# Optimization experiments

Hardware: AMD Instinct MI355X
Metric: run time of the kernel (lower is better)

The kernel has to match this reference:

```python
import jax, jax.numpy as jnp
import numpy as np
from jax import lax

EPS = 1e-5
DIM = 96      # channels = dim
KS = 96       # kernel_size == H == W
GROUPS = 8
BATCH = 4
FFN_F = 2.66

# relative index table: emb[c, i, j] = rel[c, i - j + KS - 1]
_REL_IDX = (np.arange(KS)[:, None] - np.arange(KS)[None, :] + KS - 1).reshape(-1)


def _bn(x, g, b, ax):
    """BatchNorm (training-mode batch statistics) over all axes except `ax`."""
    axes = tuple(i for i in range(x.ndim) if i != ax)
    m = x.mean(axes, keepdims=True)
    v = x.var(axes, keepdims=True)
    sh = [1] * x.ndim
    sh[ax] = -1
    return (x - m) / jnp.sqrt(v + EPS) * g.reshape(sh) + b.reshape(sh)


def _ln(x, w, b):
    """WithBias LayerNorm over channel dim of NCHW (per-pixel over C)."""
    m = x.mean(1, keepdims=True)
    v = x.var(1, keepdims=True)
    return (x - m) / jnp.sqrt(v + EPS) * w[None, :, None, None] + b[None, :, None, None]


def _axial(x, wqkv, gq, bq, rel, gs, bs, go, bo, width):
    # x: (N, C, H, W)
    xp = x.transpose(0, 2, 1, 3) if width else x.transpose(0, 3, 1, 2)
    N, Wd, C, L = xp.shape
    gp = C // GROUPS  # group_planes
    xb = xp.reshape(N * Wd, C, L)
    qkv = _bn(jnp.einsum('oc,bcl->bol', wqkv, xb), gq, bq, 1)
    qkv = qkv.reshape(N * Wd, GROUPS, 2 * gp, L)
    q, k, v = qkv[:, :, :gp // 2], qkv[:, :, gp // 2:gp], qkv[:, :, gp:]
    emb = rel[:, _REL_IDX].reshape(2 * gp, L, L)
    qe, ke, ve = emb[:gp // 2], emb[gp // 2:gp], emb[gp:]
    qk = jnp.einsum('bgci,bgcj->bgij', q, k)
    qr = jnp.einsum('bgci,cij->bgij', q, qe)
    kr = jnp.einsum('bgci,cij->bgij', k, ke).transpose(0, 1, 3, 2)
    sim = _bn(jnp.concatenate([qk, qr, kr], 1), gs, bs, 1)
    sim = sim.reshape(N * Wd, 3, GROUPS, L, L).sum(1)
    sim = jax.nn.softmax(sim, axis=3)
    sv = jnp.einsum('bgij,bgcj->bgci', sim, v)
    sve = jnp.einsum('bgij,cij->bgci', sim, ve)
    out = _bn(jnp.concatenate([sv, sve], -1).reshape(N * Wd, 2 * C, L), go, bo, 1)
    out = out.reshape(N, Wd, C, 2, L).sum(3)
    return out.transpose(0, 2, 1, 3) if width else out.transpose(0, 2, 3, 1)


def _ffn(x, win, wdw, wout):
    h = jnp.einsum('oc,bchw->bohw', win, x)
    h = lax.conv_general_dilated(h, wdw, (1, 1), 'SAME',
                                 dimension_numbers=('NCHW', 'OIHW', 'NCHW'),
                                 feature_group_count=h.shape[1])
    x1, x2 = jnp.split(h, 2, axis=1)
    return jnp.einsum('oc,bchw->bohw', wout, jax.nn.gelu(x1, approximate=False) * x2)


def setup_inputs() -> dict:
    key = jax.random.key(0)
    ks = jax.random.split(key, 8)
    dim, gp = DIM, DIM // GROUPS
    hid = int(dim * FFN_F)
    f = jax.random.normal
    d = {'x': f(ks[0], (BATCH, dim, KS, KS), jnp.float32)}
    d['ln1_w'] = jnp.ones(dim); d['ln1_b'] = jnp.zeros(dim)
    for p, i in (('h_', 1), ('w_', 2)):
        k1, k2 = jax.random.split(ks[i])
        d[p + 'wqkv'] = f(k1, (2 * dim, dim), jnp.float32) * float(np.sqrt(1.0 / dim))
        d[p + 'gqkv'] = jnp.ones(2 * dim); d[p + 'bqkv'] = jnp.zeros(2 * dim)
        d[p + 'rel'] = f(k2, (2 * gp, 2 * KS - 1), jnp.float32) * float(np.sqrt(1.0 / gp))
        d[p + 'gsim'] = jnp.ones(3 * GROUPS); d[p + 'bsim'] = jnp.zeros(3 * GROUPS)
        d[p + 'gout'] = jnp.ones(2 * dim); d[p + 'bout'] = jnp.zeros(2 * dim)
    d['ln2_w'] = jnp.ones(dim); d['ln2_b'] = jnp.zeros(dim)
    d['ffn_win'] = f(ks[3], (2 * hid, dim), jnp.float32) * float(np.sqrt(1.0 / dim))
    d['ffn_wdw'] = f(ks[4], (2 * hid, 1, 3, 3), jnp.float32) * 0.1
    d['ffn_wout'] = f(ks[5], (dim, hid), jnp.float32) * float(np.sqrt(1.0 / hid))
    return d


def reference(x, ln1_w, ln1_b,
              h_wqkv, h_gqkv, h_bqkv, h_rel, h_gsim, h_bsim, h_gout, h_bout,
              w_wqkv, w_gqkv, w_bqkv, w_rel, w_gsim, w_bsim, w_gout, w_bout,
              ln2_w, ln2_b, ffn_win, ffn_wdw, ffn_wout):
    y = _ln(x, ln1_w, ln1_b)
    y = _axial(y, h_wqkv, h_gqkv, h_bqkv, h_rel, h_gsim, h_bsim, h_gout, h_bout, False)
    y = _axial(y, w_wqkv, w_gqkv, w_bqkv, w_rel, w_gsim, w_bsim, w_gout, w_bout, True)
    x = x + y
    x = x + _ffn(_ln(x, ln2_w, ln2_b), ffn_win, ffn_wdw, ffn_wout)
    return x
```

## Files before the change

### kernel.cpp

```cpp
#include <hip/hip_runtime.h>
#include <hip/hip_bf16.h>
#include <math.h>

using bf16 = __hip_bfloat16;

#define NB 4
#define C_ 96
#define NPIX 36864
#define IMG 9216
#define CH_ST 9216
#define N_ST 884736
#define HID 255
#define EPSF 1e-5f
#define TOT 3538944

__global__ __launch_bounds__(256) void ln_kernel(const float* __restrict__ X,
                                                 float* __restrict__ Y,
                                                 const float* __restrict__ w,
                                                 const float* __restrict__ b) {
  __shared__ float red[2][4][64];
  __shared__ float wb[192];
  int tid = threadIdx.x;
  if (tid < 192) wb[tid] = (tid < 96) ? w[tid] : b[tid - 96];
  int cq = tid >> 6, px = tid & 63;
  int pix = blockIdx.x * 64 + px;
  int n = pix / IMG, p = pix % IMG;
  const float* xp = X + (long)n * N_ST + (long)(cq * 24) * CH_ST + p;
  float xr[24];
  float s = 0.f, sq = 0.f;
  #pragma unroll
  for (int k = 0; k < 24; k++) {
    float v = xp[(long)k * CH_ST];
    xr[k] = v; s += v; sq += v * v;
  }
  red[0][cq][px] = s; red[1][cq][px] = sq;
  __syncthreads();
  float S  = red[0][0][px] + red[0][1][px] + red[0][2][px] + red[0][3][px];
  float SQ = red[1][0][px] + red[1][1][px] + red[1][2][px] + red[1][3][px];
  float m = S * (1.f / C_);
  float r = rsqrtf(fmaxf(SQ * (1.f / C_) - m * m, 0.f) + EPSF);
  float* yp = Y + (long)n * N_ST + (long)(cq * 24) * CH_ST + p;
  #pragma unroll
  for (int k = 0; k < 24; k++)
    yp[(long)k * CH_ST] = (xr[k] - m) * r * wb[cq * 24 + k] + wb[96 + cq * 24 + k];
}

__global__ void trans_kernel(const float* __restrict__ Y0, float* __restrict__ Y0C) {
  __shared__ float T[32][33];
  int nc = blockIdx.z; int n = nc / C_, c = nc % C_;
  int h0 = blockIdx.x * 32, w0 = blockIdx.y * 32;
  int tx = threadIdx.x, ty = threadIdx.y;
  const float* src = Y0 + (long)n * N_ST + (long)c * CH_ST;
  for (int r = 0; r < 4; r++)
    T[ty + 8 * r][tx] = src[(h0 + ty + 8 * r) * 96 + w0 + tx];
  __syncthreads();
  float* dst = Y0C + (long)c * NPIX + (long)n * IMG;
  for (int r = 0; r < 4; r++)
    dst[(w0 + ty + 8 * r) * 96 + h0 + tx] = T[tx][ty + 8 * r];
}

template<int TM, int TN, int EPI>
__global__ __launch_bounds__(256) void gemm_kernel(
    const float* __restrict__ A, const float* __restrict__ B,
    float* __restrict__ Cout, int M, int K, int NperZ,
    long bCstride, long bZstride, int batch,
    const float* __restrict__ X1, float* __restrict__ OutF) {
  constexpr int NT = TN / 16;
  constexpr int RT = TM / 16;
  __shared__ float As[32][TM];
  __shared__ float Bs[32][TN + 4];
  const int tx = threadIdx.x, ty = threadIdx.y;
  const int tid = ty * 16 + tx;
  const int m0 = blockIdx.y * TM;
  const int q0 = blockIdx.x * TN;
  const int z  = blockIdx.z;
  const float* Bz = B + (long)z * bZstride;
  float acc[RT][NT];
  #pragma unroll
  for (int a = 0; a < RT; a++)
    #pragma unroll
    for (int b = 0; b < NT; b++) acc[a][b] = 0.f;

  for (int kk = 0; kk < K; kk += 32) {
    #pragma unroll
    for (int it = 0; it < (32 * TM) / 256; it++) {
      int i = tid + it * 256;
      int c = i / TM, r = i % TM;
      int mm = m0 + r, kc = kk + c;
      As[c][r] = (mm < M && kc < K) ? A[(long)mm * K + kc] : 0.f;
    }
    #pragma unroll
    for (int it = 0; it < (32 * TN) / 256; it++) {
      int i = tid + it * 256;
      int c = i / TN, q = i % TN;
      int kc = kk + c;
      Bs[c][q] = (kc < K) ? Bz[(long)kc * bCstride + q0 + q] : 0.f;
    }
    __syncthreads();
    for (int kc = 0; kc < 32; kc++) {
      float av[RT];
      if constexpr (RT % 4 == 0) {
        #pragma unroll
        for (int u = 0; u < RT / 4; u++) {
          float4 a4 = *(const float4*)&As[kc][ty * RT + 4 * u];
          av[4 * u] = a4.x; av[4 * u + 1] = a4.y; av[4 * u + 2] = a4.z; av[4 * u + 3] = a4.w;
        }
      } else {
        #pragma unroll
        for (int u = 0; u < RT / 2; u++) {
          float2 a2 = *(const float2*)&As[kc][ty * RT + 2 * u];
          av[2 * u] = a2.x; av[2 * u + 1] = a2.y;
        }
      }
      float bv[NT];
      #pragma unroll
      for (int v4 = 0; v4 < NT / 4; v4++) {
        float4 b4 = *(const float4*)&Bs[kc][v4 * 64 + tx * 4];
        bv[v4 * 4] = b4.x; bv[v4 * 4 + 1] = b4.y; bv[v4 * 4 + 2] = b4.z; bv[v4 * 4 + 3] = b4.w;
      }
      #pragma unroll
      for (int a = 0; a < RT; a++)
        #pragma unroll
        for (int b = 0; b < NT; b++)
          acc[a][b] = fmaf(av[a], bv[b], acc[a][b]);
    }
    __syncthreads();
  }
  const long oStride = (long)NperZ * gridDim.z;
  if (EPI == 0) {
    #pragma unroll
    for (int a = 0; a < RT; a++) {
      int mm = m0 + ty * RT + a;
      if (mm < M) {
        float* dst = Cout + (long)mm * oStride + (long)z * NperZ + q0;
        #pragma unroll
        for (int v4 = 0; v4 < NT / 4; v4++)
          *(float4*)(dst + v4 * 64 + tx * 4) =
              make_float4(acc[a][v4 * 4], acc[a][v4 * 4 + 1],
                          acc[a][v4 * 4 + 2], acc[a][v4 * 4 + 3]);
      }
    }
  } else {
    #pragma unroll
    for (int a = 0; a < RT; a++) {
      int mm = m0 + ty * RT + a;
      if (mm < M) {
        #pragma unroll
        for (int v4 = 0; v4 < NT / 4; v4++) {
          int Q = q0 + v4 * 64 + tx * 4;
          int n = batch + z + Q / IMG, p = Q % IMG;
          long base = (long)n * N_ST + (long)mm * CH_ST + p;
          #pragma unroll
          for (int b = 0; b < 4; b++)
            OutF[base + b] = acc[a][v4 * 4 + b] + X1[base + b];
        }
      }
    }
  }
}

__global__ __launch_bounds__(1024) void rowstat_kernel(const float* __restrict__ D,
                                                       const float* __restrict__ g,
                                                       const float* __restrict__ b,
                                                       float2* __restrict__ aff) {
  int o = blockIdx.x;
  const float4* p = (const float4*)(D + (long)o * NPIX);
  float s = 0.f, sq = 0.f;
  for (int i = threadIdx.x; i < NPIX / 4; i += 1024) {
    float4 v = p[i];
    s  += v.x + v.y + v.z + v.w;
    sq += v.x * v.x + v.y * v.y + v.z * v.z + v.w * v.w;
  }
  for (int off = 32; off; off >>= 1) { s += __shfl_down(s, off); sq += __shfl_down(sq, off); }
  __shared__ float ss[16], ssq[16];
  int wv = threadIdx.x >> 6, lane = threadIdx.x & 63;
  if (lane == 0) { ss[wv] = s; ssq[wv] = sq; }
  __syncthreads();
  if (threadIdx.x == 0) {
    float S = 0.f, SQ = 0.f;
    #pragma unroll
    for (int i = 0; i < 16; i++) { S += ss[i]; SQ += ssq[i]; }
    float m = S / (float)NPIX;
    float var = fmaxf(SQ / (float)NPIX - m * m, 0.f);
    float sc = g[o] * rsqrtf(var + EPSF);
    aff[o] = make_float2(sc, b[o] - m * sc);
  }
}

__global__ void relstat_kernel(const float* __restrict__ relp, float* __restrict__ tbl) {
  int i = threadIdx.x;
  if (i >= 96) return;
  int side = blockIdx.x / 27, row = blockIdx.x % 27;
  const float* base = relp + side * 6 * 191;
  float* T = tbl + side * 27 * 96;
  if (row < 6) {
    float s = 0.f;
    for (int d = 0; d < 96; d++) s += base[row * 191 + i + d];
    T[row * 96 + i] = s;
  } else {
    int p = row - 6, c = 0;
    while (p >= 6 - c) { p -= 6 - c; c++; }
    int c2 = c + p;
    float s = 0.f;
    for (int d = 0; d < 96; d++) s += base[c * 191 + i + d] * base[c2 * 191 + i + d];
    T[576 + (row - 6) * 96 + i] = s;
  }
}

__global__ __launch_bounds__(256) void simstat2_kernel(const float* __restrict__ QKV,
                                                       const float2* __restrict__ aff,
                                                       const float* __restrict__ tbl,
                                                       float* __restrict__ stats) {
  int g = blockIdx.x & 7, chunk = blockIdx.x >> 3;
  int bbg = threadIdx.x >> 5, lane = threadIdx.x & 31;
  int bb = chunk * 8 + bbg;
  const float* Aq = tbl;
  const float* Wq = tbl + 6 * 96;
  const float* Ak = tbl + 27 * 96;
  const float* Wk = tbl + 27 * 96 + 6 * 96;
  float Sq[6] = {}, Sk[6] = {}, Gq[21] = {}, Gk[21] = {};
  float lq = 0.f, lsq = 0.f, lk = 0.f, lsk = 0.f;
  #pragma unroll
  for (int ii = 0; ii < 3; ii++) {
    int i = lane + 32 * ii;
    float qv[6], kv[6];
    #pragma unroll
    for (int c = 0; c < 6; c++) {
      int oq = g * 24 + c, ok = g * 24 + 6 + c;
      float2 a = aff[oq], b2 = aff[ok];
      qv[c] = QKV[(long)oq * NPIX + bb * 96 + i] * a.x + a.y;
      kv[c] = QKV[(long)ok * NPIX + bb * 96 + i] * b2.x + b2.y;
      Sq[c] += qv[c]; Sk[c] += kv[c];
      lq = fmaf(qv[c], Aq[c * 96 + i], lq);
      lk = fmaf(kv[c], Ak[c * 96 + i], lk);
    }
    int p = 0;
    #pragma unroll
    for (int c = 0; c < 6; c++)
      #pragma unroll
      for (int c2 = c; c2 < 6; c2++, p++) {
        float f = (c == c2) ? 1.f : 2.f;
        float pq = qv[c] * qv[c2], pk = kv[c] * kv[c2];
        Gq[p] += pq; Gk[p] += pk;
        lsq = fmaf(pq * f, Wq[p * 96 + i], lsq);
        lsk = fmaf(pk * f, Wk[p * 96 + i], lsk);
      }
  }
  #pragma unroll
  for (int off = 16; off; off >>= 1) {
    #pragma unroll
    for (int c = 0; c < 6; c++) { Sq[c] += __shfl_down(Sq[c], off, 32); Sk[c] += __shfl_down(Sk[c], off, 32); }
    #pragma unroll
    for (int p = 0; p < 21; p++) { Gq[p] += __shfl_down(Gq[p], off, 32); Gk[p] += __shfl_down(Gk[p], off, 32); }
    lq += __shfl_down(lq, off, 32);  lsq += __shfl_down(lsq, off, 32);
    lk += __shfl_down(lk, off, 32);  lsk += __shfl_down(lsk, off, 32);
  }
  __shared__ float red[6];
  if (threadIdx.x < 6) red[threadIdx.x] = 0.f;
  __syncthreads();
  if (lane == 0) {
    float sqk = 0.f, sqk2 = 0.f;
    #pragma unroll
    for (int c = 0; c < 6; c++) sqk += Sq[c] * Sk[c];
    int p = 0;
    #pragma unroll
    for (int c = 0; c < 6; c++)
      #pragma unroll
      for (int c2 = c; c2 < 6; c2++, p++)
        sqk2 += ((c == c2) ? 1.f : 2.f) * Gq[p] * Gk[p];
    atomicAdd(&red[0], sqk); atomicAdd(&red[3], sqk2);
    atomicAdd(&red[1], lq);  atomicAdd(&red[4], lsq);
    atomicAdd(&red[2], lk);  atomicAdd(&red[5], lsk);
  }
  __syncthreads();
  if (threadIdx.x < 3) {
    atomicAdd(&stats[(threadIdx.x * 8 + g) * 2 + 0], red[threadIdx.x]);
    atomicAdd(&stats[(threadIdx.x * 8 + g) * 2 + 1], red[threadIdx.x + 3]);
  }
}

__global__ void simfin_kernel(const float* __restrict__ stats,
                              const float* __restrict__ gsim,
                              float* __restrict__ scale) {
  int t = threadIdx.x;
  if (t < 24) {
    float cnt = 384.f * 9216.f;
    float m = stats[t * 2] / cnt;
    float var = fmaxf(stats[t * 2 + 1] / cnt - m * m, 0.f);
    scale[t] = gsim[t] * rsqrtf(var + EPSF);
  }
}

__global__ __launch_bounds__(256) void attn_kernel(const float* __restrict__ QKV,
                                                   const float2* __restrict__ aff,
                                                   const float* __restrict__ relp,
                                                   const float* __restrict__ sscale,
                                                   float* __restrict__ OutPre) {
  int blk = blockIdx.x;
  int bb = blk >> 3, g = blk & 7;
  __shared__ float qF[6][96];
  __shared__ float kF[6][96];
  __shared__ float vF[12][96];
  __shared__ float rl[24 * 191];
  __shared__ float P[32][100];
  int tid = threadIdx.x;
  float s0 = sscale[g], s1 = sscale[8 + g], s2 = sscale[16 + g];
  for (int i = tid; i < 288; i += 256) {
    int half = i / 144, r = i % 144;
    int c = r / 24, qd = r % 24;
    int o = g * 24 + half * 6 + c;
    float2 a = aff[o];
    float4 v = *(const float4*)(QKV + (long)o * NPIX + bb * 96 + qd * 4);
    float4 w = make_float4(v.x * a.x + a.y, v.y * a.x + a.y,
                           v.z * a.x + a.y, v.w * a.x + a.y);
    if (half == 0) *(float4*)&qF[c][qd * 4] = w;
    else           *(float4*)&kF[c][qd * 4] = w;
  }
  for (int i = tid; i < 288; i += 256) {
    int c = i / 24, qd = i % 24;
    int o = g * 24 + 12 + c;
    float2 a = aff[o];
    float4 v = *(const float4*)(QKV + (long)o * NPIX + bb * 96 + qd * 4);
    *(float4*)&vF[c][qd * 4] = make_float4(v.x * a.x + a.y, v.y * a.x + a.y,
                                           v.z * a.x + a.y, v.w * a.x + a.y);
  }
  for (int i = tid; i < 1146; i += 256) {
    int e = i * 4;
    float4 v = *(const float4*)(relp + e);
    float4 w;
    w.x = v.x * ((e + 0) < 1146 ? s1 : (e + 0) < 2292 ? s2 : 1.f);
    w.y = v.y * ((e + 1) < 1146 ? s1 : (e + 1) < 2292 ? s2 : 1.f);
    w.z = v.z * ((e + 2) < 1146 ? s1 : (e + 2) < 2292 ? s2 : 1.f);
    w.w = v.w * ((e + 3) < 1146 ? s1 : (e + 3) < 2292 ? s2 : 1.f);
    *(float4*)&rl[e] = w;
  }
  __syncthreads();
  int hw = tid >> 5, l32 = tid & 31;
  float kreg[6][3];
  #pragma unroll
  for (int c = 0; c < 6; c++)
    #pragma unroll
    for (int j = 0; j < 3; j++) kreg[c][j] = kF[c][l32 * 3 + j];
  for (int iq = 0; iq < 3; iq++) {
    int i0 = iq * 32;
    {
      int til = hw * 4;
      int ti = i0 + til;
      int tj = l32 * 3;
      int d0 = ti - tj + 93;
      int e0 = tj - ti + 92;
      float ap[4][3] = {};
      #pragma unroll
      for (int c = 0; c < 6; c++) {
        float4 q4 = *(const float4*)&qF[c][ti];
        float qv[4] = {q4.x, q4.y, q4.z, q4.w};
        float kv0[3], rq[6], rk[6];
        #pragma unroll
        for (int j = 0; j < 3; j++) kv0[j] = s0 * kreg[c][j];
        #pragma unroll
        for (int u = 0; u < 6; u++) { rq[u] = rl[c * 191 + d0 + u]; rk[u] = rl[(6 + c) * 191 + e0 + u]; }
        #pragma unroll
        for (int ii = 0; ii < 4; ii++)
          #pragma unroll
          for (int jj = 0; jj < 3; jj++) {
            ap[ii][jj] = fmaf(qv[ii], kv0[jj], ap[ii][jj]);
            ap[ii][jj] = fmaf(qv[ii], rq[ii - jj + 2], ap[ii][jj]);
            ap[ii][jj] = fmaf(kreg[c][jj], rk[jj - ii + 3], ap[ii][jj]);
          }
      }
      #pragma unroll
      for (int ii = 0; ii < 4; ii++)
        #pragma unroll
        for (int jj = 0; jj < 3; jj++)
          P[til + ii][l32 * 3 + jj] = ap[ii][jj];
    }
    __syncthreads();
    {
      int wv = tid >> 6, rloc = (tid >> 3) & 7, l8 = tid & 7;
      int r = wv * 8 + rloc;
      float* Pr = &P[r][l8 * 12];
      float4 v0 = *(const float4*)(Pr);
      float4 v1 = *(const float4*)(Pr + 4);
      float4 v2 = *(const float4*)(Pr + 8);
      float mx = fmaxf(fmaxf(fmaxf(v0.x, v0.y), fmaxf(v0.z, v0.w)),
                 fmaxf(fmaxf(fmaxf(v1.x, v1.y), fmaxf(v1.z, v1.w)),
                       fmaxf(fmaxf(v2.x, v2.y), fmaxf(v2.z, v2.w))));
      #pragma unroll
      for (int off = 4; off; off >>= 1) mx = fmaxf(mx, __shfl_xor(mx, off, 8));
      v0 = make_float4(__expf(v0.x - mx), __expf(v0.y - mx), __expf(v0.z - mx), __expf(v0.w - mx));
      v1 = make_float4(__expf(v1.x - mx), __expf(v1.y - mx), __expf(v1.z - mx), __expf(v1.w - mx));
      v2 = make_float4(__expf(v2.x - mx), __expf(v2.y - mx), __expf(v2.z - mx), __expf(v2.w - mx));
      float s = v0.x + v0.y + v0.z + v0.w + v1.x + v1.y + v1.z + v1.w
              + v2.x + v2.y + v2.z + v2.w;
      #pragma unroll
      for (int off = 4; off; off >>= 1) s += __shfl_xor(s, off, 8);
      *(float4*)(Pr)     = v0;
      *(float4*)(Pr + 4) = v1;
      *(float4*)(Pr + 8) = v2;
      if (l8 == 0) P[r][96] = 1.f / s;
    }
    __syncthreads();
    {
      int orr0 = hw * 3;
      float acc3[3] = {};
      for (int jq = 0; jq < 24; jq++) {
        int j0 = jq * 4;
        float4 pv = *(const float4*)&P[l32][j0];
        #pragma unroll
        for (int u = 0; u < 3; u++) {
          int orr = orr0 + u, cc = orr >> 1;
          if ((orr & 1) == 0) {
            float4 vv = *(const float4*)&vF[cc][j0];
            acc3[u] += pv.x * vv.x + pv.y * vv.y + pv.z * vv.z + pv.w * vv.w;
          } else {
            const float* rv = &rl[(12 + cc) * 191];
            int bse = (i0 + l32) - j0 + 92;
            float f0 = rv[bse], f1 = rv[bse + 1], f2 = rv[bse + 2], f3 = rv[bse + 3];
            acc3[u] += pv.w * f0 + pv.z * f1 + pv.y * f2 + pv.x * f3;
          }
        }
      }
      float ri = P[l32][96];
      #pragma unroll
      for (int u = 0; u < 3; u++)
        OutPre[(long)(g * 24 + orr0 + u) * NPIX + bb * 96 + i0 + l32] = acc3[u] * ri;
    }
    __syncthreads();
  }
}

__global__ void apply1_kernel(const float* __restrict__ OutPre,
                              const float2* __restrict__ aff,
                              float* __restrict__ Y1) {
  __shared__ float T[32][33];
  int z = blockIdx.z; int n = z / C_, cf = z % C_;
  int h0 = blockIdx.x * 32, w0 = blockIdx.y * 32;
  int tx = threadIdx.x, ty = threadIdx.y;
  float2 a0 = aff[2 * cf], a1 = aff[2 * cf + 1];
  const float* r0 = OutPre + (long)(2 * cf) * NPIX + (long)n * IMG;
  const float* r1 = OutPre + (long)(2 * cf + 1) * NPIX + (long)n * IMG;
  for (int r = 0; r < 4; r++) {
    int w = w0 + ty + 8 * r;
    int idx = w * 96 + h0 + tx;
    T[ty + 8 * r][tx] = (r0[idx] * a0.x + a0.y) + (r1[idx] * a1.x + a1.y);
  }
  __syncthreads();
  float* dst = Y1 + (long)n * N_ST + (long)cf * CH_ST;
  for (int r = 0; r < 4; r++)
    dst[(h0 + ty + 8 * r) * 96 + w0 + tx] = T[tx][ty + 8 * r];
}

__global__ __launch_bounds__(256) void apl2_kernel(const float* __restrict__ OutPre,
                                                   const float2* __restrict__ aff,
                                                   const float* __restrict__ X,
                                                   const float* __restrict__ w,
                                                   const float* __restrict__ b,
                                                   float* __restrict__ X1out,
                                                   float* __restrict__ Yln) {
  __shared__ float red[2][4][64];
  __shared__ float2 affs[192];
  __shared__ float wb[192];
  int tid = threadIdx.x;
  if (tid < 192) { affs[tid] = aff[tid]; wb[tid] = (tid < 96) ? w[tid] : b[tid - 96]; }
  __syncthreads();
  int cq = tid >> 6, px = tid & 63;
  int pix = blockIdx.x * 64 + px;
  int n = pix / IMG, p = pix % IMG;
  const float* o0p = OutPre + (long)n * IMG + p;
  const float* xp = X + (long)n * N_ST + (long)(cq * 24) * CH_ST + p;
  float vr[24];
  float s = 0.f, sq = 0.f;
  #pragma unroll
  for (int k = 0; k < 24; k++) {
    int c = cq * 24 + k;
    float2 a0 = affs[2 * c], a1 = affs[2 * c + 1];
    float o0 = o0p[(long)(2 * c) * NPIX];
    float o1 = o0p[(long)(2 * c + 1) * NPIX];
    float v = o0 * a0.x + a0.y + o1 * a1.x + a1.y + xp[(long)k * CH_ST];
    vr[k] = v; s += v; sq += v * v;
  }
  red[0][cq][px] = s; red[1][cq][px] = sq;
  __syncthreads();
  float S  = red[0][0][px] + red[0][1][px] + red[0][2][px] + red[0][3][px];
  float SQ = red[1][0][px] + red[1][1][px] + red[1][2][px] + red[1][3][px];
  float m = S * (1.f / C_);
  float r = rsqrtf(fmaxf(SQ * (1.f / C_) - m * m, 0.f) + EPSF);
  float* x1p = X1out + (long)n * N_ST + (long)(cq * 24) * CH_ST + p;
  float* yp  = Yln   + (long)n * N_ST + (long)(cq * 24) * CH_ST + p;
  #pragma unroll
  for (int k = 0; k < 24; k++) {
    x1p[(long)k * CH_ST] = vr[k];
    int c = cq * 24 + k;
    yp[(long)k * CH_ST] = (vr[k] - m) * r * wb[c] + wb[96 + c];
  }
}

__global__ __launch_bounds__(256) void dwglu_kernel(const float* __restrict__ H,
                                                    const float* __restrict__ Wdw,
                                                    float* __restrict__ Gout) {
  int idx = blockIdx.x * 256 + threadIdx.x;
  if (idx >= HID * IMG) return;
  int c = idx / IMG;
  int p = idx % IMG, y = p / 96, x = p % 96;
  const float* h1 = H + (long)c * IMG;
  const float* h2 = H + (long)(c + HID) * IMG;
  const float* w1 = Wdw + c * 9;
  const float* w2 = Wdw + (c + HID) * 9;
  float acc1 = 0.f, acc2 = 0.f;
  #pragma unroll
  for (int dy = -1; dy <= 1; dy++) {
    int yy = y + dy; if (yy < 0 || yy >= 96) continue;
    #pragma unroll
    for (int dx = -1; dx <= 1; dx++) {
      int xx = x + dx; if (xx < 0 || xx >= 96) continue;
      int wi = (dy + 1) * 3 + dx + 1;
      acc1 = fmaf(h1[yy * 96 + xx], w1[wi], acc1);
      acc2 = fmaf(h2[yy * 96 + xx], w2[wi], acc2);
    }
  }
  float ge = 0.5f * acc1 * (1.f + erff(acc1 * 0.70710678118654752f));
  Gout[idx] = ge * acc2;
}

__global__ __launch_bounds__(256) void dwglu4_kernel(const float* __restrict__ H,
                                                     const float* __restrict__ Wdw,
                                                     float* __restrict__ Gout) {
  int idx = blockIdx.x * 256 + threadIdx.x;
  if (idx >= HID * IMG * NB) return;
  int c = idx / (IMG * NB);
  int rem = idx % (IMG * NB);
  int nb = rem / IMG;
  int p = rem % IMG, y = p / 96, x = p % 96;
  const float* h1 = H + (long)c * (IMG * NB) + (long)nb * IMG;
  const float* h2 = H + (long)(c + HID) * (IMG * NB) + (long)nb * IMG;
  const float* w1 = Wdw + c * 9;
  const float* w2 = Wdw + (c + HID) * 9;
  float acc1 = 0.f, acc2 = 0.f;
  #pragma unroll
  for (int dy = -1; dy <= 1; dy++) {
    int yy = y + dy; if (yy < 0 || yy >= 96) continue;
    #pragma unroll
    for (int dx = -1; dx <= 1; dx++) {
      int xx = x + dx; if (xx < 0 || xx >= 96) continue;
      int wi = (dy + 1) * 3 + dx + 1;
      acc1 = fmaf(h1[yy * 96 + xx], w1[wi], acc1);
      acc2 = fmaf(h2[yy * 96 + xx], w2[wi], acc2);
    }
  }
  float ge = 0.5f * acc1 * (1.f + erff(acc1 * 0.70710678118654752f));
  Gout[(long)nb * 2350080 + (long)c * IMG + p] = ge * acc2;
}

extern "C" void kernel_launch(void* const* d_in, const int* in_sizes, int n_in,
                              void* d_out, int out_size, void* d_ws, size_t ws_size,
                              hipStream_t stream) {
  const float* x       = (const float*)d_in[0];
  const float* ln1w    = (const float*)d_in[1];
  const float* ln1b    = (const float*)d_in[2];
  const float* h_wqkv  = (const float*)d_in[3];
  const float* h_gqkv  = (const float*)d_in[4];
  const float* h_bqkv  = (const float*)d_in[5];
  const float* h_rel   = (const float*)d_in[6];
  const float* h_gsim  = (const float*)d_in[7];
  const float* h_gout  = (const float*)d_in[9];
  const float* h_bout  = (const float*)d_in[10];
  const float* w_wqkv  = (const float*)d_in[11];
  const float* w_gqkv  = (const float*)d_in[12];
  const float* w_bqkv  = (const float*)d_in[13];
  const float* w_rel   = (const float*)d_in[14];
  const float* w_gsim  = (const float*)d_in[15];
  const float* w_gout  = (const float*)d_in[17];
  const float* w_bout  = (const float*)d_in[18];
  const float* ln2w    = (const float*)d_in[19];
  const float* ln2b    = (const float*)d_in[20];
  const float* ffn_win = (const float*)d_in[21];
  const float* ffn_wdw = (const float*)d_in[22];
  const float* ffn_wout= (const float*)d_in[23];
  float* out = (float*)d_out;

  float* ws = (float*)d_ws;
  float* P = ws;
  float* Q = ws + 3538944;
  float* R = ws + 7077888;
  float* S = ws + 14155776;
  float* Gall = R;
  float* Hbuf = ws + 16478208;
  const size_t base_need = (21233664ull + 8192ull) * 4ull;
  const size_t big_need  = (35278848ull + 8192ull) * 4ull;
  if (ws_size < base_need) return;
  const bool batched = (ws_size >= big_need);
  float* stats = batched ? (ws + 35278848) : (ws + 21233664);

  float2* qkv_aff = (float2*)stats;
  float2* out_aff = (float2*)(stats + 384);
  float*  sim_st  = stats + 768;
  float*  sim_sc  = stats + 864;
  float*  tbl     = stats + 1024;

  hipMemsetAsync(sim_st, 0, 96 * sizeof(float), stream);

  dim3 b256(256), b1616(16, 16), b328(32, 8);

  ln_kernel<<<576, b256, 0, stream>>>(x, P, ln1w, ln1b);
  trans_kernel<<<dim3(3, 3, 384), b328, 0, stream>>>(P, Q);

  gemm_kernel<96, 128, 0><<<dim3(288, 2, 1), b1616, 0, stream>>>(h_wqkv, Q, R,
      192, 96, 36864, 36864L, 0L, 0, nullptr, nullptr);
  rowstat_kernel<<<192, 1024, 0, stream>>>(R, h_gqkv, h_bqkv, qkv_aff);
  relstat_kernel<<<54, 96, 0, stream>>>(h_rel, tbl);
  simstat2_kernel<<<384, b256, 0, stream>>>(R, qkv_aff, tbl, sim_st);
  simfin_kernel<<<1, 32, 0, stream>>>(sim_st, h_gsim, sim_sc);
  attn_kernel<<<3072, b256, 0, stream>>>(R, qkv_aff, h_rel, sim_sc, S);
  rowstat_kernel<<<192, 1024, 0, stream>>>(S, h_gout, h_bout, out_aff);
  apply1_kernel<<<dim3(3, 3, 384), b328, 0, stream>>>(S, out_aff, P);

  gemm_kernel<96, 128, 0><<<dim3(72, 2, 4), b1616, 0, stream>>>(w_wqkv, P, R,
      192, 96, 9216, 9216L, 884736L, 0, nullptr, nullptr);
  rowstat_kernel<<<192, 1024, 0, stream>>>(R, w_gqkv, w_bqkv, qkv_aff);
  relstat_kernel<<<54, 96, 0, stream>>>(w_rel, tbl);
  simstat2_kernel<<<384, b256, 0, stream>>>(R, qkv_aff, tbl, sim_st + 48);
  simfin_kernel<<<1, 32, 0, stream>>>(sim_st + 48, w_gsim, sim_sc + 24);
  attn_kernel<<<3072, b256, 0, stream>>>(R, qkv_aff, w_rel, sim_sc + 24, S);
  rowstat_kernel<<<192, 1024, 0, stream>>>(S, w_gout, w_bout, out_aff);
  apl2_kernel<<<576, b256, 0, stream>>>(S, out_aff, x, ln2w, ln2b, P, Q);

  if (batched) {
    gemm_kernel<128, 64, 0><<<dim3(144, 4, 4), b1616, 0, stream>>>(ffn_win, Q, Hbuf,
        510, 96, 9216, 9216L, 884736L, 0, nullptr, nullptr);
    dwglu4_kernel<<<36720, b256, 0, stream>>>(Hbuf, ffn_wdw, Gall);
  } else {
    for (int n = 0; n < NB; n++) {
      gemm_kernel<128, 64, 0><<<dim3(144, 4, 1), b1616, 0, stream>>>(ffn_win, Q + (long)n * N_ST, Hbuf,
          510, 96, 9216, 9216L, 0L, 0, nullptr, nullptr);
      dwglu_kernel<<<9180, b256, 0, stream>>>(Hbuf, ffn_wdw, Gall + (long)n * 2350080);
    }
  }
  gemm_kernel<96, 64, 1><<<dim3(144, 1, 4), b1616, 0, stream>>>(ffn_wout, Gall, nullptr,
      96, 255, 9216, 9216L, 2350080L, 0, P, out);
}
```

Measured before the change: 852.9 us.

## Fuse QKV batchnorm statistics into GEMM epilogue and drop finalize kernels

The QKV GEMM epilogue now reduces per-row sum and sum of squares across lanes and atomically accumulates them, which removes the two rowstat passes over the 192x36864 QKV buffer. The simstat and attention kernels compute the BN affine and similarity scales inline, so the simfin kernels are gone as well. apply1 zeroes the sum buffer between the two axial passes, and a single memset clears the stats area. The cost is extra shuffles and global atomics in the GEMM, plus a one-pass variance formula that is less numerically robust.

```diff
diff --git a/kernel.cpp b/kernel.cpp
--- a/kernel.cpp
+++ b/kernel.cpp
@@ -13,6 +13,7 @@
 #define HID 255
 #define EPSF 1e-5f
 #define TOT 3538944
+#define RNPIX (1.f / 36864.f)
 
 __global__ __launch_bounds__(256) void ln_kernel(const float* __restrict__ X,
                                                  float* __restrict__ Y,
@@ -59,12 +60,13 @@
     dst[(w0 + ty + 8 * r) * 96 + h0 + tx] = T[tx][ty + 8 * r];
 }
 
-template<int TM, int TN, int EPI>
+template<int TM, int TN, int EPI, int STATS>
 __global__ __launch_bounds__(256) void gemm_kernel(
     const float* __restrict__ A, const float* __restrict__ B,
     float* __restrict__ Cout, int M, int K, int NperZ,
     long bCstride, long bZstride, int batch,
-    const float* __restrict__ X1, float* __restrict__ OutF) {
+    const float* __restrict__ X1, float* __restrict__ OutF,
+    float* __restrict__ rsum) {
   constexpr int NT = TN / 16;
   constexpr int RT = TM / 16;
   __shared__ float As[32][TM];
@@ -154,6 +156,23 @@
           for (int b = 0; b < 4; b++)
             OutF[base + b] = acc[a][v4 * 4 + b] + X1[base + b];
         }
+      }
+    }
+  }
+  if (STATS) {
+    #pragma unroll
+    for (int a = 0; a < RT; a++) {
+      int mm = m0 + ty * RT + a;
+      float s = 0.f, sq = 0.f;
+      #pragma unroll
+      for (int b = 0; b < NT; b++) { float v = acc[a][b]; s += v; sq += v * v; }
+      #pragma unroll
+      for (int off = 8; off; off >>= 1) {
+        s += __shfl_down(s, off, 16); sq += __shfl_down(sq, off, 16);
+      }
+      if (tx == 0 && mm < M) {
+        atomicAdd(&rsum[mm], s);
+        atomicAdd(&rsum[192 + mm], sq);
       }
     }
   }
@@ -208,7 +227,9 @@
 }
 
 __global__ __launch_bounds__(256) void simstat2_kernel(const float* __restrict__ QKV,
-                                                       const float2* __restrict__ aff,
+                                                       const float* __restrict__ qsum,
+                                                       const float* __restrict__ gq,
+                                                       const float* __restrict__ bq,
                                                        const float* __restrict__ tbl,
                                                        float* __restrict__ stats) {
   int g = blockIdx.x & 7, chunk = blockIdx.x >> 3;
@@ -218,6 +239,17 @@
   const float* Wq = tbl + 6 * 96;
   const float* Ak = tbl + 27 * 96;
   const float* Wk = tbl + 27 * 96 + 6 * 96;
+  float qa[6], qb[6], ka[6], kb[6];
+  #pragma unroll
+  for (int c = 0; c < 6; c++) {
+    int oq = g * 24 + c, ok = g * 24 + 6 + c;
+    float m1 = qsum[oq] * RNPIX;
+    float v1 = fmaxf(qsum[192 + oq] * RNPIX - m1 * m1, 0.f);
+    qa[c] = gq[oq] * rsqrtf(v1 + EPSF); qb[c] = bq[oq] - m1 * qa[c];
+    float m2 = qsum[ok] * RNPIX;
+    float v2 = fmaxf(qsum[192 + ok] * RNPIX - m2 * m2, 0.f);
+    ka[c] = gq[ok] * rsqrtf(v2 + EPSF); kb[c] = bq[ok] - m2 * ka[c];
+  }
   float Sq[6] = {}, Sk[6] = {}, Gq[21] = {}, Gk[21] = {};
   float lq = 0.f, lsq = 0.f, lk = 0.f, lsk = 0.f;
   #pragma unroll
@@ -227,9 +259,8 @@
     #pragma unroll
     for (int c = 0; c < 6; c++) {
       int oq = g * 24 + c, ok = g * 24 + 6 + c;
-      float2 a = aff[oq], b2 = aff[ok];
-      qv[c] = QKV[(long)oq * NPIX + bb * 96 + i] * a.x + a.y;
-      kv[c] = QKV[(long)ok * NPIX + bb * 96 + i] * b2.x + b2.y;
+      qv[c] = QKV[(long)oq * NPIX + bb * 96 + i] * qa[c] + qb[c];
+      kv[c] = QKV[(long)ok * NPIX + bb * 96 + i] * ka[c] + kb[c];
       Sq[c] += qv[c]; Sk[c] += kv[c];
       lq = fmaf(qv[c], Aq[c * 96 + i], lq);
       lk = fmaf(kv[c], Ak[c * 96 + i], lk);
@@ -279,22 +310,13 @@
   }
 }
 
-__global__ void simfin_kernel(const float* __restrict__ stats,
-                              const float* __restrict__ gsim,
-                              float* __restrict__ scale) {
-  int t = threadIdx.x;
-  if (t < 24) {
-    float cnt = 384.f * 9216.f;
-    float m = stats[t * 2] / cnt;
-    float var = fmaxf(stats[t * 2 + 1] / cnt - m * m, 0.f);
-    scale[t] = gsim[t] * rsqrtf(var + EPSF);
-  }
-}
-
 __global__ __launch_bounds__(256) void attn_kernel(const float* __restrict__ QKV,
-                                                   const float2* __restrict__ aff,
+                                                   const float* __restrict__ qsum,
+                                                   const float* __restrict__ gq,
+                                                   const float* __restrict__ bq,
                                                    const float* __restrict__ relp,
-                                                   const float* __restrict__ sscale,
+                                                   const float* __restrict__ simst,
+                                                   const float* __restrict__ gsim,
                                                    float* __restrict__ OutPre) {
   int blk = blockIdx.x;
   int bb = blk >> 3, g = blk & 7;
@@ -303,13 +325,28 @@
   __shared__ float vF[12][96];
   __shared__ float rl[24 * 191];
   __shared__ float P[32][100];
+  __shared__ float2 aff_s[24];
   int tid = threadIdx.x;
-  float s0 = sscale[g], s1 = sscale[8 + g], s2 = sscale[16 + g];
+  const float rc = 1.f / 3538944.f;
+  float m0s = simst[2 * g] * rc;
+  float s0 = gsim[g] * rsqrtf(fmaxf(simst[2 * g + 1] * rc - m0s * m0s, 0.f) + EPSF);
+  float m1s = simst[2 * (8 + g)] * rc;
+  float s1 = gsim[8 + g] * rsqrtf(fmaxf(simst[2 * (8 + g) + 1] * rc - m1s * m1s, 0.f) + EPSF);
+  float m2s = simst[2 * (16 + g)] * rc;
+  float s2 = gsim[16 + g] * rsqrtf(fmaxf(simst[2 * (16 + g) + 1] * rc - m2s * m2s, 0.f) + EPSF);
+  if (tid < 24) {
+    int o = g * 24 + tid;
+    float m = qsum[o] * RNPIX;
+    float var = fmaxf(qsum[192 + o] * RNPIX - m * m, 0.f);
+    float sc = gq[o] * rsqrtf(var + EPSF);
+    aff_s[tid] = make_float2(sc, bq[o] - m * sc);
+  }
+  __syncthreads();
   for (int i = tid; i < 288; i += 256) {
     int half = i / 144, r = i % 144;
     int c = r / 24, qd = r % 24;
+    float2 a = aff_s[half * 6 + c];
     int o = g * 24 + half * 6 + c;
-    float2 a = aff[o];
     float4 v = *(const float4*)(QKV + (long)o * NPIX + bb * 96 + qd * 4);
     float4 w = make_float4(v.x * a.x + a.y, v.y * a.x + a.y,
                            v.z * a.x + a.y, v.w * a.x + a.y);
@@ -318,8 +355,8 @@
   }
   for (int i = tid; i < 288; i += 256) {
     int c = i / 24, qd = i % 24;
+    float2 a = aff_s[12 + c];
     int o = g * 24 + 12 + c;
-    float2 a = aff[o];
     float4 v = *(const float4*)(QKV + (long)o * NPIX + bb * 96 + qd * 4);
     *(float4*)&vF[c][qd * 4] = make_float4(v.x * a.x + a.y, v.y * a.x + a.y,
                                            v.z * a.x + a.y, v.w * a.x + a.y);
@@ -431,11 +468,15 @@
 
 __global__ void apply1_kernel(const float* __restrict__ OutPre,
                               const float2* __restrict__ aff,
+                              float* __restrict__ qsum,
                               float* __restrict__ Y1) {
   __shared__ float T[32][33];
+  int tx = threadIdx.x, ty = threadIdx.y;
+  if (blockIdx.x == 0 && blockIdx.y == 0 && blockIdx.z == 0) {
+    for (int t = ty * 32 + tx; t < 384; t += 256) qsum[t] = 0.f;
+  }
   int z = blockIdx.z; int n = z / C_, cf = z % C_;
   int h0 = blockIdx.x * 32, w0 = blockIdx.y * 32;
-  int tx = threadIdx.x, ty = threadIdx.y;
   float2 a0 = aff[2 * cf], a1 = aff[2 * cf + 1];
   const float* r0 = OutPre + (long)(2 * cf) * NPIX + (long)n * IMG;
   const float* r1 = OutPre + (long)(2 * cf + 1) * NPIX + (long)n * IMG;
@@ -591,50 +632,45 @@
   const bool batched = (ws_size >= big_need);
   float* stats = batched ? (ws + 35278848) : (ws + 21233664);
 
-  float2* qkv_aff = (float2*)stats;
+  float*  qkv_sum = stats;
   float2* out_aff = (float2*)(stats + 384);
   float*  sim_st  = stats + 768;
-  float*  sim_sc  = stats + 864;
   float*  tbl     = stats + 1024;
 
-  hipMemsetAsync(sim_st, 0, 96 * sizeof(float), stream);
+  hipMemsetAsync(stats, 0, 8192 * sizeof(float), stream);
 
   dim3 b256(256), b1616(16, 16), b328(32, 8);
 
   ln_kernel<<<576, b256, 0, stream>>>(x, P, ln1w, ln1b);
   trans_kernel<<<dim3(3, 3, 384), b328, 0, stream>>>(P, Q);
 
-  gemm_kernel<96, 128, 0><<<dim3(288, 2, 1), b1616, 0, stream>>>(h_wqkv, Q, R,
-      192, 96, 36864, 36864L, 0L, 0, nullptr, nullptr);
-  rowstat_kernel<<<192, 1024, 0, stream>>>(R, h_gqkv, h_bqkv, qkv_aff);
+  gemm_kernel<96, 128, 0, 1><<<dim3(288, 2, 1), b1616, 0, stream>>>(h_wqkv, Q, R,
+      192, 96, 36864, 36864L, 0L, 0, nullptr, nullptr, qkv_sum);
   relstat_kernel<<<54, 96, 0, stream>>>(h_rel, tbl);
-  simstat2_kernel<<<384, b256, 0, stream>>>(R, qkv_aff, tbl, sim_st);
-  simfin_kernel<<<1, 32, 0, stream>>>(sim_st, h_gsim, sim_sc);
-  attn_kernel<<<3072, b256, 0, stream>>>(R, qkv_aff, h_rel, sim_sc, S);
+  simstat2_kernel<<<384, b256, 0, stream>>>(R, qkv_sum, h_gqkv, h_bqkv, tbl, sim_st);
+  attn_kernel<<<3072, b256, 0, stream>>>(R, qkv_sum, h_gqkv, h_bqkv, h_rel, sim_st, h_gsim, S);
   rowstat_kernel<<<192, 1024, 0, stream>>>(S, h_gout, h_bout, out_aff);
-  apply1_kernel<<<dim3(3, 3, 384), b328, 0, stream>>>(S, out_aff, P);
-
-  gemm_kernel<96, 128, 0><<<dim3(72, 2, 4), b1616, 0, stream>>>(w_wqkv, P, R,
-      192, 96, 9216, 9216L, 884736L, 0, nullptr, nullptr);
-  rowstat_kernel<<<192, 1024, 0, stream>>>(R, w_gqkv, w_bqkv, qkv_aff);
+  apply1_kernel<<<dim3(3, 3, 384), b328, 0, stream>>>(S, out_aff, qkv_sum, P);
+
+  gemm_kernel<96, 128, 0, 1><<<dim3(72, 2, 4), b1616, 0, stream>>>(w_wqkv, P, R,
+      192, 96, 9216, 9216L, 884736L, 0, nullptr, nullptr, qkv_sum);
   relstat_kernel<<<54, 96, 0, stream>>>(w_rel, tbl);
-  simstat2_kernel<<<384, b256, 0, stream>>>(R, qkv_aff, tbl, sim_st + 48);
-  simfin_kernel<<<1, 32, 0, stream>>>(sim_st + 48, w_gsim, sim_sc + 24);
-  attn_kernel<<<3072, b256, 0, stream>>>(R, qkv_aff, w_rel, sim_sc + 24, S);
+  simstat2_kernel<<<384, b256, 0, stream>>>(R, qkv_sum, w_gqkv, w_bqkv, tbl, sim_st + 48);
+  attn_kernel<<<3072, b256, 0, stream>>>(R, qkv_sum, w_gqkv, w_bqkv, w_rel, sim_st + 48, w_gsim, S);
   rowstat_kernel<<<192, 1024, 0, stream>>>(S, w_gout, w_bout, out_aff);
   apl2_kernel<<<576, b256, 0, stream>>>(S, out_aff, x, ln2w, ln2b, P, Q);
 
   if (batched) {
-    gemm_kernel<128, 64, 0><<<dim3(144, 4, 4), b1616, 0, stream>>>(ffn_win, Q, Hbuf,
-        510, 96, 9216, 9216L, 884736L, 0, nullptr, nullptr);
+    gemm_kernel<128, 64, 0, 0><<<dim3(144, 4, 4), b1616, 0, stream>>>(ffn_win, Q, Hbuf,
+        510, 96, 9216, 9216L, 884736L, 0, nullptr, nullptr, nullptr);
     dwglu4_kernel<<<36720, b256, 0, stream>>>(Hbuf, ffn_wdw, Gall);
   } else {
     for (int n = 0; n < NB; n++) {
-      gemm_kernel<128, 64, 0><<<dim3(144, 4, 1), b1616, 0, stream>>>(ffn_win, Q + (long)n * N_ST, Hbuf,
-          510, 96, 9216, 9216L, 0L, 0, nullptr, nullptr);
+      gemm_kernel<128, 64, 0, 0><<<dim3(144, 4, 1), b1616, 0, stream>>>(ffn_win, Q + (long)n * N_ST, Hbuf,
+          510, 96, 9216, 9216L, 0L, 0, nullptr, nullptr, nullptr);
       dwglu_kernel<<<9180, b256, 0, stream>>>(Hbuf, ffn_wdw, Gall + (long)n * 2350080);
     }
   }
-  gemm_kernel<96, 64, 1><<<dim3(144, 1, 4), b1616, 0, stream>>>(ffn_wout, Gall, nullptr,
-      96, 255, 9216, 9216L, 2350080L, 0, P, out);
-}
+  gemm_kernel<96, 64, 1, 0><<<dim3(144, 1, 4), b1616, 0, stream>>>(ffn_wout, Gall, nullptr,
+      96, 255, 9216, 9216L, 2350080L, 0, P, out, nullptr);
+}
```

Result: slower. 967.2 us (+13.4%).
